# Kernel optimization log

Hardware: AMD Instinct MI355X
Metric: run time of the kernel (lower is better)

The kernel has to match this reference:

```python
import jax, jax.numpy as jnp
import numpy as np

NUM_GRAPHS = 256
N_NODES = 100000
N_EDGES = 1200000
NODE_DIM = 64
NUM_LAYERS = 3
R_HID = 128
R_OUT = 32


def setup_inputs() -> dict:
    key = jax.random.key(0)
    ks = jax.random.split(key, 10)
    x = jax.random.normal(ks[0], (N_NODES, NODE_DIM), dtype=jnp.float32)
    src = jax.random.randint(ks[1], (N_EDGES,), 0, N_NODES)
    dst = jax.random.randint(ks[2], (N_EDGES,), 0, N_NODES)
    graph_ids = jnp.sort(jax.random.randint(ks[3], (N_NODES,), 0, NUM_GRAPHS))
    s = 1.0 / np.sqrt(NODE_DIM)
    gin_W = jax.random.normal(ks[4], (NUM_LAYERS, NODE_DIM, NODE_DIM), dtype=jnp.float32) * s
    gin_b = jnp.zeros((NUM_LAYERS, NODE_DIM), dtype=jnp.float32)
    eps = jnp.zeros((NUM_LAYERS,), dtype=jnp.float32)  # learnable GIN epsilon
    in_dim = NODE_DIM * NUM_LAYERS
    r_W1 = jax.random.normal(ks[5], (in_dim, R_HID), dtype=jnp.float32) / np.sqrt(in_dim)
    r_b1 = jnp.zeros((R_HID,), dtype=jnp.float32)
    r_W2 = jax.random.normal(ks[6], (R_HID, R_OUT), dtype=jnp.float32) / np.sqrt(R_HID)
    r_b2 = jnp.zeros((R_OUT,), dtype=jnp.float32)
    return {"x": x, "gin_W": gin_W, "gin_b": gin_b, "eps": eps,
            "r_W1": r_W1, "r_b1": r_b1, "r_W2": r_W2, "r_b2": r_b2,
            "src": src, "dst": dst, "graph_ids": graph_ids}


def reference(x, gin_W, gin_b, eps, r_W1, r_b1, r_W2, r_b2, src, dst, graph_ids):
    n = x.shape[0]
    h = x
    hs = []
    for l in range(NUM_LAYERS):  # fixed small layer loop
        # neighbor sum aggregation: scatter-add messages h[src] into dst
        agg = jax.ops.segment_sum(h[src], dst, num_segments=n)  # [N, D]
        h = jax.nn.relu(((1.0 + eps[l]) * h + agg) @ gin_W[l] + gin_b[l])
        hs.append(h)
    H = jnp.stack(hs, axis=1)  # [N, L, D]
    # dgl.sum_nodes per layer output == ragged segment-sum over graph ids
    g = jax.ops.segment_sum(H, graph_ids, num_segments=NUM_GRAPHS)  # [B, L, D]
    g = g.reshape(NUM_GRAPHS, -1)  # [B, L*D]
    # readout MLP (2 layers)
    out = jax.nn.relu(g @ r_W1 + r_b1) @ r_W2 + r_b2
    return out
```

## Files before the change

kernel.cpp:

```cpp
#include <hip/hip_runtime.h>


#define SPLIT 16
#define NBLK 512
#define BS 512

typedef unsigned short ushort_t;
typedef __bf16 v8bf __attribute__((ext_vector_type(8)));
typedef float v4f __attribute__((ext_vector_type(4)));

__device__ __forceinline__ float h2f_lo(unsigned int v) {
    return (float)__builtin_bit_cast(_Float16, (unsigned short)(v & 0xffffu));
}
__device__ __forceinline__ float h2f_hi(unsigned int v) {
    return (float)__builtin_bit_cast(_Float16, (unsigned short)(v >> 16));
}
__device__ __forceinline__ unsigned int f2h(float f) {
    return (unsigned int)__builtin_bit_cast(unsigned short, (_Float16)f);
}

__global__ __launch_bounds__(256) void pre_kernel(
        const int* __restrict__ dst, int* __restrict__ cnt2d,
        int E, int nbkt, int ebpb,
        const float* __restrict__ x, ushort_t* __restrict__ xh, int n4, int castBlocks,
        const float* __restrict__ W, ushort_t* __restrict__ whi,
        ushort_t* __restrict__ wlo, int wtotal) {
    __shared__ int lcnt[256];
    int t = threadIdx.x;
    int blk = blockIdx.x;
    if (blk < NBLK) {
        lcnt[t] = 0;
        __syncthreads();
        int base = blk * ebpb;
        int end = min(base + ebpb, E);
        for (int i = base + t; i < end; i += 256)
            atomicAdd(&lcnt[dst[i] >> 9], 1);
        __syncthreads();
        if (t < nbkt) cnt2d[(size_t)blk * nbkt + t] = lcnt[t];
    } else if (blk < NBLK + castBlocks) {
        int i = (blk - NBLK) * 256 + t;
        if (i < n4) {
            float4 v = ((const float4*)x)[i];
            uint2 p;
            p.x = f2h(v.x) | (f2h(v.y) << 16);
            p.y = f2h(v.z) | (f2h(v.w) << 16);
            ((uint2*)xh)[i] = p;
        }
    } else {
        int i = (blk - NBLK - castBlocks) * 256 + t;
        if (i < wtotal) {
            int l = i >> 12, r = i & 4095;
            int n = r >> 6, k = r & 63;
            float w = W[l * 4096 + k * 64 + n];
            __bf16 h = (__bf16)w;
            float rem = w - (float)h;
            whi[i] = __builtin_bit_cast(ushort_t, h);
            wlo[i] = __builtin_bit_cast(ushort_t, (__bf16)rem);
        }
    }
}

__global__ __launch_bounds__(256) void colscan_kernel(
        const int* __restrict__ cnt2d, int* __restrict__ blkoff,
        int* __restrict__ btot, int nbkt) {
    __shared__ int sh[256];
    int b = blockIdx.x, t = threadIdx.x;
    int i0 = 2 * t, i1 = 2 * t + 1;
    int v0 = cnt2d[(size_t)i0 * nbkt + b];
    int v1 = cnt2d[(size_t)i1 * nbkt + b];
    int pair = v0 + v1;
    sh[t] = pair;
    __syncthreads();
    for (int off = 1; off < 256; off <<= 1) {
        int u = (t >= off) ? sh[t - off] : 0;
        __syncthreads();
        sh[t] += u;
        __syncthreads();
    }
    int ex = sh[t] - pair;
    blkoff[(size_t)b * NBLK + i0] = ex;
    blkoff[(size_t)b * NBLK + i1] = ex + v0;
    if (t == 255) btot[b] = sh[255];
}

__global__ __launch_bounds__(256) void bucket_base_kernel(
        const int* __restrict__ btot, int* __restrict__ bbase,
        int* __restrict__ offsets, int nbkt, int N, int E) {
    __shared__ int sh[256];
    int t = threadIdx.x;
    int v = (t < nbkt) ? btot[t] : 0;
    sh[t] = v;
    __syncthreads();
    for (int off = 1; off < 256; off <<= 1) {
        int u = (t >= off) ? sh[t - off] : 0;
        __syncthreads();
        sh[t] += u;
        __syncthreads();
    }
    if (t < nbkt) bbase[t] = sh[t] - v;
    if (t == 0) { bbase[nbkt] = E; offsets[N] = E; }
}

__global__ __launch_bounds__(256) void bucket_scatter_kernel(
        const int* __restrict__ src, const int* __restrict__ dst,
        const int* __restrict__ bbase, const int* __restrict__ blkoff,
        unsigned int* __restrict__ bkt, int E, int nbkt, int ebpb) {
    __shared__ int lbase[256];
    __shared__ int lrank[256];
    int t = threadIdx.x;
    if (t < nbkt) lbase[t] = bbase[t] + blkoff[(size_t)t * NBLK + blockIdx.x];
    lrank[t] = 0;
    __syncthreads();
    int base = blockIdx.x * ebpb;
    int end = min(base + ebpb, E);
    for (int i = base + t; i < end; i += 256) {
        int d = dst[i];
        int b = d >> 9;
        int r = atomicAdd(&lrank[b], 1);
        bkt[lbase[b] + r] = ((unsigned int)src[i] << 9) | (unsigned int)(d & (BS - 1));
    }
}

__global__ __launch_bounds__(256) void csr_build_kernel(
        const unsigned int* __restrict__ bkt, const int* __restrict__ bbase,
        int* __restrict__ offsets, int* __restrict__ csr, int N, int nbkt) {
    __shared__ int cnt[BS];
    __shared__ int rank[BS];
    __shared__ int sh[256];
    int b = blockIdx.x, t = threadIdx.x;
    cnt[t] = 0; cnt[t + 256] = 0;
    rank[t] = 0; rank[t + 256] = 0;
    __syncthreads();
    int base = bbase[b], end = bbase[b + 1];
    for (int i = base + t; i < end; i += 256)
        atomicAdd(&cnt[bkt[i] & (BS - 1)], 1);
    __syncthreads();
    int i0 = 2 * t, i1 = 2 * t + 1;
    int v0 = cnt[i0], v1 = cnt[i1];
    int pair = v0 + v1;
    sh[t] = pair;
    __syncthreads();
    for (int off = 1; off < 256; off <<= 1) {
        int u = (t >= off) ? sh[t - off] : 0;
        __syncthreads();
        sh[t] += u;
        __syncthreads();
    }
    int ex = sh[t] - pair;
    __syncthreads();
    cnt[i0] = ex;
    cnt[i1] = ex + v0;
    __syncthreads();
    int d0 = (b << 9) + i0;
    if (d0 <= N) offsets[d0] = base + cnt[i0];
    int d1 = (b << 9) + i1;
    if (d1 <= N) offsets[d1] = base + cnt[i1];
    for (int i = base + t; i < end; i += 256) {
        unsigned int v = bkt[i];
        int dl = v & (BS - 1);
        int r = atomicAdd(&rank[dl], 1);
        csr[base + cnt[dl] + r] = (int)(v >> 9);
    }
}

#define CONSUME_NODE(kk, dgv, e0v, buf, sf) { \
    float ax = 0.f, ay = 0.f, az = 0.f, aw = 0.f; \
    _Pragma("unroll") \
    for (int j = 0; j < 6; ++j) { \
        if (g + 4 * j < (dgv)) { \
            ax += h2f_lo(buf[j].x); ay += h2f_hi(buf[j].x); \
            az += h2f_lo(buf[j].y); aw += h2f_hi(buf[j].y); } } \
    if ((dgv) > 24) {                    \
        int dc_ = min((dgv), 64); \
        for (int j = 24 + g; j < dc_; j += 4) { \
            int s_ = __shfl(idxa[kk], j, 64); \
            uint2 v_ = hp2[(size_t)s_ * 16 + sl]; \
            ax += h2f_lo(v_.x); ay += h2f_hi(v_.x); \
            az += h2f_lo(v_.y); aw += h2f_hi(v_.y); } \
        for (int j = 64 + g; j < (dgv); j += 4) {    \
            int s_ = csr[(e0v) + j]; \
            uint2 v_ = hp2[(size_t)s_ * 16 + sl]; \
            ax += h2f_lo(v_.x); ay += h2f_hi(v_.x); \
            az += h2f_lo(v_.y); aw += h2f_hi(v_.y); } } \
    ax += __shfl_xor(ax, 16, 64); ax += __shfl_xor(ax, 32, 64); \
    ay += __shfl_xor(ay, 16, 64); ay += __shfl_xor(ay, 32, 64); \
    az += __shfl_xor(az, 16, 64); az += __shfl_xor(az, 32, 64); \
    aw += __shfl_xor(aw, 16, 64); aw += __shfl_xor(aw, 32, 64); \
    if (tile * 16 + (kk) < N) { \
        ax = fmaf(eps1, h2f_lo(sf.x), ax); ay = fmaf(eps1, h2f_hi(sf.x), ay); \
        az = fmaf(eps1, h2f_lo(sf.y), az); aw = fmaf(eps1, h2f_hi(sf.y), aw); } \
    if (g == 0) { \
        float4 r4_; r4_.x = ax; r4_.y = ay; r4_.z = az; r4_.w = aw; \
        *(float4*)&myrows[(kk) * 64 + sl * 4] = r4_; } }

__global__ __launch_bounds__(256, 4) void layer_kernel(
        const ushort_t* __restrict__ hin, ushort_t* __restrict__ hout,
        const int* __restrict__ offsets, const int* __restrict__ csr,
        const ushort_t* __restrict__ wt_hi, const ushort_t* __restrict__ wt_lo,
        const float* __restrict__ gin_b, const float* __restrict__ eps_arr,
        int layer, int N, int E) {
    __shared__ float rows[4 * 16 * 64];
    int t = threadIdx.x;
    int wv = t >> 6, lane = t & 63;
    int tile = blockIdx.x * 4 + wv;
    if (tile * 16 >= N) return;
    float* myrows = rows + wv * 16 * 64;
    const uint2* hp2 = (const uint2*)hin;
    float eps1 = 1.0f + eps_arr[layer];

    int g  = lane >> 4;
    int sl = lane & 15;

    int off_l = offsets[min(tile * 16 + lane, N)];
    int e0a[17];
    #pragma unroll
    for (int k = 0; k < 17; ++k)
        e0a[k] = __builtin_amdgcn_readlane(off_l, k);

    int idxa[16];
    #pragma unroll
    for (int k = 0; k < 16; ++k) {
        int dg_ = e0a[k + 1] - e0a[k];
        int v_ = csr[min(e0a[k] + lane, E - 1)];
        idxa[k] = (lane < dg_) ? v_ : 0;
    }

    #pragma unroll
    for (int kb = 0; kb < 8; ++kb) {
        const int k = kb * 2;
        int e0A = e0a[k],     dgA = e0a[k + 1] - e0a[k];
        int e0B = e0a[k + 1], dgB = e0a[k + 2] - e0a[k + 1];
        uint2 b[6], c[6];
        #pragma unroll
        for (int j = 0; j < 6; ++j) {
            int p = g + 4 * j;
            int s = (p < dgA) ? __shfl(idxa[k], p, 64) : 0;
            b[j] = hp2[(size_t)s * 16 + sl];
        }
        #pragma unroll
        for (int j = 0; j < 6; ++j) {
            int p = g + 4 * j;
            int s = (p < dgB) ? __shfl(idxa[k + 1], p, 64) : 0;
            c[j] = hp2[(size_t)s * 16 + sl];
        }
        uint2 sfA = hp2[(size_t)min(tile * 16 + k,     N - 1) * 16 + sl];
        uint2 sfB = hp2[(size_t)min(tile * 16 + k + 1, N - 1) * 16 + sl];
        __builtin_amdgcn_sched_barrier(0);
        CONSUME_NODE(k,     dgA, e0A, b, sfA)
        CONSUME_NODE(k + 1, dgB, e0B, c, sfB)
    }

    int c2 = lane & 15;
    int q  = lane >> 4;
    int node16 = tile * 16 + c2;

    const ushort_t* Whi = wt_hi + layer * 4096;
    const ushort_t* Wlo = wt_lo + layer * 4096;
    const float*    bl  = gin_b + layer * 64;

    v8bf bhi[2], blo2[2];
    #pragma unroll
    for (int kt = 0; kt < 2; ++kt) {
        float4 f0 = *(float4*)&myrows[c2 * 64 + kt * 32 + q * 8];
        float4 f1 = *(float4*)&myrows[c2 * 64 + kt * 32 + q * 8 + 4];
        float xs[8] = {f0.x, f0.y, f0.z, f0.w, f1.x, f1.y, f1.z, f1.w};
        #pragma unroll
        for (int j = 0; j < 8; ++j) {
            __bf16 h = (__bf16)xs[j];
            bhi[kt][j] = h;
            blo2[kt][j] = (__bf16)(xs[j] - (float)h);
        }
    }

    #pragma unroll
    for (int mt = 0; mt < 4; ++mt) {
        v4f acc = {0.f, 0.f, 0.f, 0.f};
        #pragma unroll
        for (int kt = 0; kt < 2; ++kt) {
            int dim = mt * 16 + c2;
            size_t off = (size_t)dim * 64 + kt * 32 + q * 8;
            v8bf ah = __builtin_bit_cast(v8bf, *(const uint4*)(Whi + off));
            v8bf al = __builtin_bit_cast(v8bf, *(const uint4*)(Wlo + off));
            acc = __builtin_amdgcn_mfma_f32_16x16x32_bf16(ah, bhi[kt],  acc, 0, 0, 0);
            acc = __builtin_amdgcn_mfma_f32_16x16x32_bf16(ah, blo2[kt], acc, 0, 0, 0);
            acc = __builtin_amdgcn_mfma_f32_16x16x32_bf16(al, bhi[kt],  acc, 0, 0, 0);
        }
        float4 bv = ((const float4*)(bl + mt * 16))[q];
        float o0 = fmaxf(acc[0] + bv.x, 0.f);
        float o1 = fmaxf(acc[1] + bv.y, 0.f);
        float o2 = fmaxf(acc[2] + bv.z, 0.f);
        float o3 = fmaxf(acc[3] + bv.w, 0.f);
        uint2 pk;
        pk.x = f2h(o0) | (f2h(o1) << 16);
        pk.y = f2h(o2) | (f2h(o3) << 16);
        if (node16 < N)
            *(uint2*)(hout + (size_t)node16 * 64 + mt * 16 + q * 4) = pk;
    }
}

__global__ __launch_bounds__(192) void readout_part_kernel(
        const ushort_t* __restrict__ H, const int* __restrict__ gids,
        float* __restrict__ gpart, int N) {
    int graph = blockIdx.x / SPLIT;
    int sp    = blockIdx.x % SPLIT;
    int lo = 0, hi = N;
    while (lo < hi) { int mid = (lo + hi) >> 1; if (gids[mid] < graph) lo = mid + 1; else hi = mid; }
    int start = lo;
    int lo2 = start, hi2 = N;
    while (lo2 < hi2) { int mid = (lo2 + hi2) >> 1; if (gids[mid] < graph + 1) lo2 = mid + 1; else hi2 = mid; }
    int end = lo2;
    int t = threadIdx.x;
    int l = t >> 6, d = t & 63;
    float acc = 0.0f;
    int cnt = end - start;
    if (cnt > 0) {
        int per = (cnt + SPLIT - 1) / SPLIT;
        int cs = start + sp * per;
        int ce = min(cs + per, end);
        const ushort_t* Hl = H + (size_t)l * N * 64;
        for (int n = cs; n < ce; ++n)
            acc += (float)__builtin_bit_cast(_Float16, Hl[(size_t)n * 64 + d]);
    }
    gpart[(size_t)(graph * SPLIT + sp) * 192 + t] = acc;
}

__global__ __launch_bounds__(192) void mlp_kernel(
        const float* __restrict__ gpart,
        const float* __restrict__ W1, const float* __restrict__ b1,
        const float* __restrict__ W2, const float* __restrict__ b2,
        float* __restrict__ out) {
    __shared__ float gr[192];
    __shared__ float hid[128];
    int graph = blockIdx.x;
    int t = threadIdx.x;
    float a = 0.f;
    #pragma unroll
    for (int sp = 0; sp < SPLIT; ++sp)
        a += gpart[(size_t)(graph * SPLIT + sp) * 192 + t];
    gr[t] = a;
    __syncthreads();
    if (t < 128) {
        float s = b1[t];
        for (int k = 0; k < 192; ++k) s = fmaf(gr[k], W1[k * 128 + t], s);
        hid[t] = fmaxf(s, 0.0f);
    }
    __syncthreads();
    if (t < 32) {
        float s = b2[t];
        for (int k = 0; k < 128; ++k) s = fmaf(hid[k], W2[k * 32 + t], s);
        out[graph * 32 + t] = s;
    }
}

extern "C" void kernel_launch(void* const* d_in, const int* in_sizes, int n_in,
                              void* d_out, int out_size, void* d_ws, size_t ws_size,
                              hipStream_t stream) {
    const float* x     = (const float*)d_in[0];
    const float* gin_W = (const float*)d_in[1];
    const float* gin_b = (const float*)d_in[2];
    const float* eps   = (const float*)d_in[3];
    const float* r_W1  = (const float*)d_in[4];
    const float* r_b1  = (const float*)d_in[5];
    const float* r_W2  = (const float*)d_in[6];
    const float* r_b2  = (const float*)d_in[7];
    const int*   src   = (const int*)d_in[8];
    const int*   dst   = (const int*)d_in[9];
    const int*   gids  = (const int*)d_in[10];

    int N = in_sizes[0] / 64;
    int E = in_sizes[8];
    int B = out_size / 32;

    int nbkt = (N + BS - 1) / BS;
    int ebpb = (E + NBLK - 1) / NBLK;
    int n4 = N * 64 / 4;
    int castBlocks = (n4 + 255) / 256;
    int wtotal = 3 * 4096;
    int prepBlocks = (wtotal + 255) / 256;

    int* ws       = (int*)d_ws;
    float* gpart  = (float*)ws;
    int* cnt2d    = ws + (size_t)B * SPLIT * 192;
    int* blkoff   = cnt2d + (size_t)NBLK * nbkt;
    int* btot     = blkoff + (size_t)nbkt * NBLK;
    int* bbase    = btot + nbkt;
    int* offsets  = bbase + (nbkt + 1);
    unsigned int* bkt = (unsigned int*)(offsets + (N + 1));
    int* csr      = (int*)(bkt + E);
    size_t w      = (size_t)(csr + E - ws);
    w = (w + 15) & ~(size_t)15;
    ushort_t* xh  = (ushort_t*)(ws + w);
    ushort_t* H   = xh + (size_t)N * 64;
    ushort_t* whi = H + 3 * (size_t)N * 64;
    ushort_t* wlo = whi + 3 * 4096;

    pre_kernel<<<NBLK + castBlocks + prepBlocks, 256, 0, stream>>>(
        dst, cnt2d, E, nbkt, ebpb, x, xh, n4, castBlocks, gin_W, whi, wlo, wtotal);
    colscan_kernel<<<nbkt, 256, 0, stream>>>(cnt2d, blkoff, btot, nbkt);
    bucket_base_kernel<<<1, 256, 0, stream>>>(btot, bbase, offsets, nbkt, N, E);
    bucket_scatter_kernel<<<NBLK, 256, 0, stream>>>(src, dst, bbase, blkoff, bkt, E, nbkt, ebpb);
    csr_build_kernel<<<nbkt, 256, 0, stream>>>(bkt, bbase, offsets, csr, N, nbkt);

    int lbk = (N + 63) / 64;
    ushort_t* H0 = H;
    ushort_t* H1 = H + (size_t)N * 64;
    ushort_t* H2 = H + 2 * (size_t)N * 64;

    layer_kernel<<<lbk, 256, 0, stream>>>(xh, H0, offsets, csr, whi, wlo, gin_b, eps, 0, N, E);
    layer_kernel<<<lbk, 256, 0, stream>>>(H0, H1, offsets, csr, whi, wlo, gin_b, eps, 1, N, E);
    layer_kernel<<<lbk, 256, 0, stream>>>(H1, H2, offsets, csr, whi, wlo, gin_b, eps, 2, N, E);

    readout_part_kernel<<<B * SPLIT, 192, 0, stream>>>(H, gids, gpart, N);
    mlp_kernel<<<B, 192, 0, stream>>>(gpart, r_W1, r_b1, r_W2, r_b2, (float*)d_out);
}
```

Before: 307.3 us.

## Fuse CSR build stages into one cooperative kernel and vectorize readout

Merges the five preprocessing kernels (bucket count with casts, column scan, bucket base scan, bucket scatter, per-bucket CSR build) into a single cooperative kernel. The stages are separated by grid-wide syncs, and each block recomputes the small bucket-base scan instead of running a separate single-block kernel. This removes several launches and their serialization gaps, at the cost of needing all 512 blocks to be co-resident and paying for the grid barriers. The readout partial-sum kernel now loads 8-byte vectors covering four nodes at a time per wavefront and combines lanes with cross-lane shuffles, instead of scalar half-precision loads.

```diff
diff --git a/kernel.cpp b/kernel.cpp
--- a/kernel.cpp
+++ b/kernel.cpp
@@ -1,5 +1,8 @@
 #include <hip/hip_runtime.h>
-
+#include <hip/hip_cooperative_groups.h>
+
+
+namespace cg = cooperative_groups;
 
 #define SPLIT 16
 #define NBLK 512
@@ -19,147 +22,147 @@
     return (unsigned int)__builtin_bit_cast(unsigned short, (_Float16)f);
 }
 
-__global__ __launch_bounds__(256) void pre_kernel(
-        const int* __restrict__ dst, int* __restrict__ cnt2d,
-        int E, int nbkt, int ebpb,
-        const float* __restrict__ x, ushort_t* __restrict__ xh, int n4, int castBlocks,
-        const float* __restrict__ W, ushort_t* __restrict__ whi,
-        ushort_t* __restrict__ wlo, int wtotal) {
-    __shared__ int lcnt[256];
+__global__ __launch_bounds__(256) void prep_coop_kernel(
+        const int* __restrict__ src, const int* __restrict__ dst,
+        const float* __restrict__ x, const float* __restrict__ W,
+        int* __restrict__ cnt2d, int* __restrict__ btot,
+        int* __restrict__ blkoff, unsigned int* __restrict__ bkt,
+        int* __restrict__ csr, int* __restrict__ offsets,
+        ushort_t* __restrict__ xh, ushort_t* __restrict__ whi,
+        ushort_t* __restrict__ wlo,
+        int N, int E, int nbkt, int ebpb, int n4, int wtotal) {
+    cg::grid_group grid = cg::this_grid();
+    __shared__ int shA[BS];
+    __shared__ int shB[BS];
+    __shared__ int shS[256];
     int t = threadIdx.x;
     int blk = blockIdx.x;
-    if (blk < NBLK) {
-        lcnt[t] = 0;
-        __syncthreads();
+
+    shA[t] = 0;
+    __syncthreads();
+    {
         int base = blk * ebpb;
         int end = min(base + ebpb, E);
         for (int i = base + t; i < end; i += 256)
-            atomicAdd(&lcnt[dst[i] >> 9], 1);
-        __syncthreads();
-        if (t < nbkt) cnt2d[(size_t)blk * nbkt + t] = lcnt[t];
-    } else if (blk < NBLK + castBlocks) {
-        int i = (blk - NBLK) * 256 + t;
-        if (i < n4) {
-            float4 v = ((const float4*)x)[i];
-            uint2 p;
-            p.x = f2h(v.x) | (f2h(v.y) << 16);
-            p.y = f2h(v.z) | (f2h(v.w) << 16);
-            ((uint2*)xh)[i] = p;
-        }
-    } else {
-        int i = (blk - NBLK - castBlocks) * 256 + t;
-        if (i < wtotal) {
-            int l = i >> 12, r = i & 4095;
-            int n = r >> 6, k = r & 63;
-            float w = W[l * 4096 + k * 64 + n];
-            __bf16 h = (__bf16)w;
-            float rem = w - (float)h;
-            whi[i] = __builtin_bit_cast(ushort_t, h);
-            wlo[i] = __builtin_bit_cast(ushort_t, (__bf16)rem);
-        }
-    }
-}
-
-__global__ __launch_bounds__(256) void colscan_kernel(
-        const int* __restrict__ cnt2d, int* __restrict__ blkoff,
-        int* __restrict__ btot, int nbkt) {
-    __shared__ int sh[256];
-    int b = blockIdx.x, t = threadIdx.x;
-    int i0 = 2 * t, i1 = 2 * t + 1;
-    int v0 = cnt2d[(size_t)i0 * nbkt + b];
-    int v1 = cnt2d[(size_t)i1 * nbkt + b];
-    int pair = v0 + v1;
-    sh[t] = pair;
+            atomicAdd(&shA[dst[i] >> 9], 1);
+    }
     __syncthreads();
-    for (int off = 1; off < 256; off <<= 1) {
-        int u = (t >= off) ? sh[t - off] : 0;
-        __syncthreads();
-        sh[t] += u;
-        __syncthreads();
-    }
-    int ex = sh[t] - pair;
-    blkoff[(size_t)b * NBLK + i0] = ex;
-    blkoff[(size_t)b * NBLK + i1] = ex + v0;
-    if (t == 255) btot[b] = sh[255];
-}
-
-__global__ __launch_bounds__(256) void bucket_base_kernel(
-        const int* __restrict__ btot, int* __restrict__ bbase,
-        int* __restrict__ offsets, int nbkt, int N, int E) {
-    __shared__ int sh[256];
-    int t = threadIdx.x;
-    int v = (t < nbkt) ? btot[t] : 0;
-    sh[t] = v;
-    __syncthreads();
-    for (int off = 1; off < 256; off <<= 1) {
-        int u = (t >= off) ? sh[t - off] : 0;
-        __syncthreads();
-        sh[t] += u;
-        __syncthreads();
-    }
-    if (t < nbkt) bbase[t] = sh[t] - v;
-    if (t == 0) { bbase[nbkt] = E; offsets[N] = E; }
-}
-
-__global__ __launch_bounds__(256) void bucket_scatter_kernel(
-        const int* __restrict__ src, const int* __restrict__ dst,
-        const int* __restrict__ bbase, const int* __restrict__ blkoff,
-        unsigned int* __restrict__ bkt, int E, int nbkt, int ebpb) {
-    __shared__ int lbase[256];
-    __shared__ int lrank[256];
-    int t = threadIdx.x;
-    if (t < nbkt) lbase[t] = bbase[t] + blkoff[(size_t)t * NBLK + blockIdx.x];
-    lrank[t] = 0;
-    __syncthreads();
-    int base = blockIdx.x * ebpb;
-    int end = min(base + ebpb, E);
-    for (int i = base + t; i < end; i += 256) {
-        int d = dst[i];
-        int b = d >> 9;
-        int r = atomicAdd(&lrank[b], 1);
-        bkt[lbase[b] + r] = ((unsigned int)src[i] << 9) | (unsigned int)(d & (BS - 1));
-    }
-}
-
-__global__ __launch_bounds__(256) void csr_build_kernel(
-        const unsigned int* __restrict__ bkt, const int* __restrict__ bbase,
-        int* __restrict__ offsets, int* __restrict__ csr, int N, int nbkt) {
-    __shared__ int cnt[BS];
-    __shared__ int rank[BS];
-    __shared__ int sh[256];
-    int b = blockIdx.x, t = threadIdx.x;
-    cnt[t] = 0; cnt[t + 256] = 0;
-    rank[t] = 0; rank[t + 256] = 0;
-    __syncthreads();
-    int base = bbase[b], end = bbase[b + 1];
-    for (int i = base + t; i < end; i += 256)
-        atomicAdd(&cnt[bkt[i] & (BS - 1)], 1);
-    __syncthreads();
-    int i0 = 2 * t, i1 = 2 * t + 1;
-    int v0 = cnt[i0], v1 = cnt[i1];
-    int pair = v0 + v1;
-    sh[t] = pair;
-    __syncthreads();
-    for (int off = 1; off < 256; off <<= 1) {
-        int u = (t >= off) ? sh[t - off] : 0;
-        __syncthreads();
-        sh[t] += u;
-        __syncthreads();
-    }
-    int ex = sh[t] - pair;
-    __syncthreads();
-    cnt[i0] = ex;
-    cnt[i1] = ex + v0;
-    __syncthreads();
-    int d0 = (b << 9) + i0;
-    if (d0 <= N) offsets[d0] = base + cnt[i0];
-    int d1 = (b << 9) + i1;
-    if (d1 <= N) offsets[d1] = base + cnt[i1];
-    for (int i = base + t; i < end; i += 256) {
-        unsigned int v = bkt[i];
-        int dl = v & (BS - 1);
-        int r = atomicAdd(&rank[dl], 1);
-        csr[base + cnt[dl] + r] = (int)(v >> 9);
+    if (t < nbkt) cnt2d[(size_t)blk * nbkt + t] = shA[t];
+    for (int i = blk * 256 + t; i < n4; i += NBLK * 256) {
+        float4 v = ((const float4*)x)[i];
+        uint2 p;
+        p.x = f2h(v.x) | (f2h(v.y) << 16);
+        p.y = f2h(v.z) | (f2h(v.w) << 16);
+        ((uint2*)xh)[i] = p;
+    }
+    for (int i = blk * 256 + t; i < wtotal; i += NBLK * 256) {
+        int l = i >> 12, r = i & 4095;
+        int n = r >> 6, k = r & 63;
+        float w = W[l * 4096 + k * 64 + n];
+        __bf16 h = (__bf16)w;
+        float rem = w - (float)h;
+        whi[i] = __builtin_bit_cast(ushort_t, h);
+        wlo[i] = __builtin_bit_cast(ushort_t, (__bf16)rem);
+    }
+    __threadfence();
+    grid.sync();
+
+    if (blk < nbkt) {
+        int b = blk;
+        int i0 = 2 * t, i1 = 2 * t + 1;
+        int v0 = cnt2d[(size_t)i0 * nbkt + b];
+        int v1 = cnt2d[(size_t)i1 * nbkt + b];
+        int pair = v0 + v1;
+        shS[t] = pair;
+        __syncthreads();
+        for (int off = 1; off < 256; off <<= 1) {
+            int u = (t >= off) ? shS[t - off] : 0;
+            __syncthreads();
+            shS[t] += u;
+            __syncthreads();
+        }
+        int ex = shS[t] - pair;
+        blkoff[(size_t)b * NBLK + i0] = ex;
+        blkoff[(size_t)b * NBLK + i1] = ex + v0;
+        if (t == 255) btot[b] = shS[255];
+    }
+    __threadfence();
+    grid.sync();
+
+    {
+        int v = (t < nbkt) ? btot[t] : 0;
+        shS[t] = v;
+        __syncthreads();
+        for (int off = 1; off < 256; off <<= 1) {
+            int u = (t >= off) ? shS[t - off] : 0;
+            __syncthreads();
+            shS[t] += u;
+            __syncthreads();
+        }
+        int bbase_ex = shS[t] - v;
+        if (t < nbkt) shA[t] = bbase_ex + blkoff[(size_t)t * NBLK + blk];
+        shB[t] = 0;
+        __syncthreads();
+        int base = blk * ebpb;
+        int end = min(base + ebpb, E);
+        for (int i = base + t; i < end; i += 256) {
+            int d = dst[i];
+            int b = d >> 9;
+            int r = atomicAdd(&shB[b], 1);
+            bkt[shA[b] + r] = ((unsigned int)src[i] << 9) | (unsigned int)(d & (BS - 1));
+        }
+    }
+    __threadfence();
+    grid.sync();
+
+    if (blk < nbkt) {
+        int b = blk;
+        int v = (t < nbkt) ? btot[t] : 0;
+        shS[t] = v;
+        __syncthreads();
+        for (int off = 1; off < 256; off <<= 1) {
+            int u = (t >= off) ? shS[t - off] : 0;
+            __syncthreads();
+            shS[t] += u;
+            __syncthreads();
+        }
+        shB[t] = shS[t] - v;
+        __syncthreads();
+        int base = shB[b];
+        int end = base + btot[b];
+        __syncthreads();
+        shA[t] = 0; shA[t + 256] = 0;
+        shB[t] = 0; shB[t + 256] = 0;
+        __syncthreads();
+        for (int i = base + t; i < end; i += 256)
+            atomicAdd(&shA[bkt[i] & (BS - 1)], 1);
+        __syncthreads();
+        int i0 = 2 * t, i1 = 2 * t + 1;
+        int v0 = shA[i0], v1 = shA[i1];
+        int pair = v0 + v1;
+        shS[t] = pair;
+        __syncthreads();
+        for (int off = 1; off < 256; off <<= 1) {
+            int u = (t >= off) ? shS[t - off] : 0;
+            __syncthreads();
+            shS[t] += u;
+            __syncthreads();
+        }
+        int ex = shS[t] - pair;
+        __syncthreads();
+        shA[i0] = ex;
+        shA[i1] = ex + v0;
+        __syncthreads();
+        int d0 = (b << 9) + i0;
+        if (d0 <= N) offsets[d0] = base + shA[i0];
+        int d1 = (b << 9) + i1;
+        if (d1 <= N) offsets[d1] = base + shA[i1];
+        for (int i = base + t; i < end; i += 256) {
+            unsigned int v2 = bkt[i];
+            int dl = v2 & (BS - 1);
+            int r = atomicAdd(&shB[dl], 1);
+            csr[base + shA[dl] + r] = (int)(v2 >> 9);
+        }
     }
 }
 
@@ -310,18 +313,30 @@
     while (lo2 < hi2) { int mid = (lo2 + hi2) >> 1; if (gids[mid] < graph + 1) lo2 = mid + 1; else hi2 = mid; }
     int end = lo2;
     int t = threadIdx.x;
-    int l = t >> 6, d = t & 63;
-    float acc = 0.0f;
+    int l = t >> 6, lane = t & 63;
+    int nd  = lane >> 4;
+    int slp = lane & 15;
+    float a0 = 0.f, a1 = 0.f, a2 = 0.f, a3 = 0.f;
     int cnt = end - start;
     if (cnt > 0) {
         int per = (cnt + SPLIT - 1) / SPLIT;
         int cs = start + sp * per;
         int ce = min(cs + per, end);
-        const ushort_t* Hl = H + (size_t)l * N * 64;
-        for (int n = cs; n < ce; ++n)
-            acc += (float)__builtin_bit_cast(_Float16, Hl[(size_t)n * 64 + d]);
-    }
-    gpart[(size_t)(graph * SPLIT + sp) * 192 + t] = acc;
+        const uint2* Hl = (const uint2*)(H + (size_t)l * N * 64);
+        for (int n = cs + nd; n < ce; n += 4) {
+            uint2 v = Hl[(size_t)n * 16 + slp];
+            a0 += h2f_lo(v.x); a1 += h2f_hi(v.x);
+            a2 += h2f_lo(v.y); a3 += h2f_hi(v.y);
+        }
+    }
+    a0 += __shfl_xor(a0, 16, 64); a0 += __shfl_xor(a0, 32, 64);
+    a1 += __shfl_xor(a1, 16, 64); a1 += __shfl_xor(a1, 32, 64);
+    a2 += __shfl_xor(a2, 16, 64); a2 += __shfl_xor(a2, 32, 64);
+    a3 += __shfl_xor(a3, 16, 64); a3 += __shfl_xor(a3, 32, 64);
+    if (lane < 16) {
+        float4 r4; r4.x = a0; r4.y = a1; r4.z = a2; r4.w = a3;
+        *(float4*)&gpart[(size_t)(graph * SPLIT + sp) * 192 + l * 64 + slp * 4] = r4;
+    }
 }
 
 __global__ __launch_bounds__(192) void mlp_kernel(
@@ -374,9 +389,7 @@
     int nbkt = (N + BS - 1) / BS;
     int ebpb = (E + NBLK - 1) / NBLK;
     int n4 = N * 64 / 4;
-    int castBlocks = (n4 + 255) / 256;
     int wtotal = 3 * 4096;
-    int prepBlocks = (wtotal + 255) / 256;
 
     int* ws       = (int*)d_ws;
     float* gpart  = (float*)ws;
@@ -394,12 +407,16 @@
     ushort_t* whi = H + 3 * (size_t)N * 64;
     ushort_t* wlo = whi + 3 * 4096;
 
-    pre_kernel<<<NBLK + castBlocks + prepBlocks, 256, 0, stream>>>(
-        dst, cnt2d, E, nbkt, ebpb, x, xh, n4, castBlocks, gin_W, whi, wlo, wtotal);
-    colscan_kernel<<<nbkt, 256, 0, stream>>>(cnt2d, blkoff, btot, nbkt);
-    bucket_base_kernel<<<1, 256, 0, stream>>>(btot, bbase, offsets, nbkt, N, E);
-    bucket_scatter_kernel<<<NBLK, 256, 0, stream>>>(src, dst, bbase, blkoff, bkt, E, nbkt, ebpb);
-    csr_build_kernel<<<nbkt, 256, 0, stream>>>(bkt, bbase, offsets, csr, N, nbkt);
+    {
+        void* args[] = {
+            (void*)&src, (void*)&dst, (void*)&x, (void*)&gin_W,
+            (void*)&cnt2d, (void*)&btot, (void*)&blkoff, (void*)&bkt,
+            (void*)&csr, (void*)&offsets, (void*)&xh, (void*)&whi, (void*)&wlo,
+            (void*)&N, (void*)&E, (void*)&nbkt, (void*)&ebpb,
+            (void*)&n4, (void*)&wtotal };
+        hipLaunchCooperativeKernel((void*)prep_coop_kernel,
+                                   dim3(NBLK), dim3(256), args, 0, stream);
+    }
 
     int lbk = (N + 63) / 64;
     ushort_t* H0 = H;
```

New measurement: 639.0 us. 2.08x slower.

## Replace per-block column scan with global atomic bucket cursors; vectorize readout loads

Applied to the files above, without the earlier changes.

Bucket totals are now accumulated with global atomics in pre_kernel, which removes the per-block count matrix and the colscan kernel. The scatter kernel recounts its own edges and claims a contiguous range per bucket through an atomic cursor, so the edge order inside each bucket is no longer deterministic. This adds a memset and a second pass over dst in exchange for one less kernel launch. Separately, the readout partial-sum kernel reads four fp16 values per thread as uint2 across four node lanes and reduces them with wave shuffles, giving wider and more coalesced loads.

```diff
diff --git a/kernel.cpp b/kernel.cpp
--- a/kernel.cpp
+++ b/kernel.cpp
@@ -20,7 +20,7 @@
 }
 
 __global__ __launch_bounds__(256) void pre_kernel(
-        const int* __restrict__ dst, int* __restrict__ cnt2d,
+        const int* __restrict__ dst, int* __restrict__ btot,
         int E, int nbkt, int ebpb,
         const float* __restrict__ x, ushort_t* __restrict__ xh, int n4, int castBlocks,
         const float* __restrict__ W, ushort_t* __restrict__ whi,
@@ -36,7 +36,7 @@
         for (int i = base + t; i < end; i += 256)
             atomicAdd(&lcnt[dst[i] >> 9], 1);
         __syncthreads();
-        if (t < nbkt) cnt2d[(size_t)blk * nbkt + t] = lcnt[t];
+        if (t < nbkt && lcnt[t]) atomicAdd(&btot[t], lcnt[t]);
     } else if (blk < NBLK + castBlocks) {
         int i = (blk - NBLK) * 256 + t;
         if (i < n4) {
@@ -60,16 +60,14 @@
     }
 }
 
-__global__ __launch_bounds__(256) void colscan_kernel(
-        const int* __restrict__ cnt2d, int* __restrict__ blkoff,
-        int* __restrict__ btot, int nbkt) {
+__global__ __launch_bounds__(256) void bucket_base_kernel(
+        const int* __restrict__ btot, int* __restrict__ bbase,
+        int* __restrict__ cursor, int* __restrict__ offsets,
+        int nbkt, int N, int E) {
     __shared__ int sh[256];
-    int b = blockIdx.x, t = threadIdx.x;
-    int i0 = 2 * t, i1 = 2 * t + 1;
-    int v0 = cnt2d[(size_t)i0 * nbkt + b];
-    int v1 = cnt2d[(size_t)i1 * nbkt + b];
-    int pair = v0 + v1;
-    sh[t] = pair;
+    int t = threadIdx.x;
+    int v = (t < nbkt) ? btot[t] : 0;
+    sh[t] = v;
     __syncthreads();
     for (int off = 1; off < 256; off <<= 1) {
         int u = (t >= off) ? sh[t - off] : 0;
@@ -77,42 +75,28 @@
         sh[t] += u;
         __syncthreads();
     }
-    int ex = sh[t] - pair;
-    blkoff[(size_t)b * NBLK + i0] = ex;
-    blkoff[(size_t)b * NBLK + i1] = ex + v0;
-    if (t == 255) btot[b] = sh[255];
-}
-
-__global__ __launch_bounds__(256) void bucket_base_kernel(
-        const int* __restrict__ btot, int* __restrict__ bbase,
-        int* __restrict__ offsets, int nbkt, int N, int E) {
-    __shared__ int sh[256];
-    int t = threadIdx.x;
-    int v = (t < nbkt) ? btot[t] : 0;
-    sh[t] = v;
-    __syncthreads();
-    for (int off = 1; off < 256; off <<= 1) {
-        int u = (t >= off) ? sh[t - off] : 0;
-        __syncthreads();
-        sh[t] += u;
-        __syncthreads();
-    }
-    if (t < nbkt) bbase[t] = sh[t] - v;
+    int ex = sh[t] - v;
+    if (t < nbkt) { bbase[t] = ex; cursor[t] = ex; }
     if (t == 0) { bbase[nbkt] = E; offsets[N] = E; }
 }
 
 __global__ __launch_bounds__(256) void bucket_scatter_kernel(
         const int* __restrict__ src, const int* __restrict__ dst,
-        const int* __restrict__ bbase, const int* __restrict__ blkoff,
-        unsigned int* __restrict__ bkt, int E, int nbkt, int ebpb) {
+        int* __restrict__ cursor, unsigned int* __restrict__ bkt,
+        int E, int nbkt, int ebpb) {
+    __shared__ int lcnt[256];
     __shared__ int lbase[256];
     __shared__ int lrank[256];
     int t = threadIdx.x;
-    if (t < nbkt) lbase[t] = bbase[t] + blkoff[(size_t)t * NBLK + blockIdx.x];
-    lrank[t] = 0;
+    lcnt[t] = 0; lrank[t] = 0;
     __syncthreads();
     int base = blockIdx.x * ebpb;
     int end = min(base + ebpb, E);
+    for (int i = base + t; i < end; i += 256)
+        atomicAdd(&lcnt[dst[i] >> 9], 1);
+    __syncthreads();
+    if (t < nbkt && lcnt[t]) lbase[t] = atomicAdd(&cursor[t], lcnt[t]);
+    __syncthreads();
     for (int i = base + t; i < end; i += 256) {
         int d = dst[i];
         int b = d >> 9;
@@ -310,18 +294,30 @@
     while (lo2 < hi2) { int mid = (lo2 + hi2) >> 1; if (gids[mid] < graph + 1) lo2 = mid + 1; else hi2 = mid; }
     int end = lo2;
     int t = threadIdx.x;
-    int l = t >> 6, d = t & 63;
-    float acc = 0.0f;
+    int l = t >> 6, lane = t & 63;
+    int nd  = lane >> 4;
+    int slp = lane & 15;
+    float a0 = 0.f, a1 = 0.f, a2 = 0.f, a3 = 0.f;
     int cnt = end - start;
     if (cnt > 0) {
         int per = (cnt + SPLIT - 1) / SPLIT;
         int cs = start + sp * per;
         int ce = min(cs + per, end);
-        const ushort_t* Hl = H + (size_t)l * N * 64;
-        for (int n = cs; n < ce; ++n)
-            acc += (float)__builtin_bit_cast(_Float16, Hl[(size_t)n * 64 + d]);
-    }
-    gpart[(size_t)(graph * SPLIT + sp) * 192 + t] = acc;
+        const uint2* Hl = (const uint2*)(H + (size_t)l * N * 64);
+        for (int n = cs + nd; n < ce; n += 4) {
+            uint2 v = Hl[(size_t)n * 16 + slp];
+            a0 += h2f_lo(v.x); a1 += h2f_hi(v.x);
+            a2 += h2f_lo(v.y); a3 += h2f_hi(v.y);
+        }
+    }
+    a0 += __shfl_xor(a0, 16, 64); a0 += __shfl_xor(a0, 32, 64);
+    a1 += __shfl_xor(a1, 16, 64); a1 += __shfl_xor(a1, 32, 64);
+    a2 += __shfl_xor(a2, 16, 64); a2 += __shfl_xor(a2, 32, 64);
+    a3 += __shfl_xor(a3, 16, 64); a3 += __shfl_xor(a3, 32, 64);
+    if (lane < 16) {
+        float4 r4; r4.x = a0; r4.y = a1; r4.z = a2; r4.w = a3;
+        *(float4*)&gpart[(size_t)(graph * SPLIT + sp) * 192 + l * 64 + slp * 4] = r4;
+    }
 }
 
 __global__ __launch_bounds__(192) void mlp_kernel(
@@ -380,10 +376,9 @@
 
     int* ws       = (int*)d_ws;
     float* gpart  = (float*)ws;
-    int* cnt2d    = ws + (size_t)B * SPLIT * 192;
-    int* blkoff   = cnt2d + (size_t)NBLK * nbkt;
-    int* btot     = blkoff + (size_t)nbkt * NBLK;
-    int* bbase    = btot + nbkt;
+    int* btot     = ws + (size_t)B * SPLIT * 192;
+    int* cursor   = btot + nbkt;
+    int* bbase    = cursor + nbkt;
     int* offsets  = bbase + (nbkt + 1);
     unsigned int* bkt = (unsigned int*)(offsets + (N + 1));
     int* csr      = (int*)(bkt + E);
@@ -394,11 +389,11 @@
     ushort_t* whi = H + 3 * (size_t)N * 64;
     ushort_t* wlo = whi + 3 * 4096;
 
+    hipMemsetAsync(btot, 0, nbkt * sizeof(int), stream);
     pre_kernel<<<NBLK + castBlocks + prepBlocks, 256, 0, stream>>>(
-        dst, cnt2d, E, nbkt, ebpb, x, xh, n4, castBlocks, gin_W, whi, wlo, wtotal);
-    colscan_kernel<<<nbkt, 256, 0, stream>>>(cnt2d, blkoff, btot, nbkt);
-    bucket_base_kernel<<<1, 256, 0, stream>>>(btot, bbase, offsets, nbkt, N, E);
-    bucket_scatter_kernel<<<NBLK, 256, 0, stream>>>(src, dst, bbase, blkoff, bkt, E, nbkt, ebpb);
+        dst, btot, E, nbkt, ebpb, x, xh, n4, castBlocks, gin_W, whi, wlo, wtotal);
+    bucket_base_kernel<<<1, 256, 0, stream>>>(btot, bbase, cursor, offsets, nbkt, N, E);
+    bucket_scatter_kernel<<<NBLK, 256, 0, stream>>>(src, dst, cursor, bkt, E, nbkt, ebpb);
     csr_build_kernel<<<nbkt, 256, 0, stream>>>(bkt, bbase, offsets, csr, N, nbkt);
 
     int lbk = (N + 63) / 64;
```

Measured after the change: 312.8 us. About the same (+1.8%).
